# Performance work log

Hardware: AMD Instinct MI355X
Metric: run time of the kernel (lower is better)

## Reference

```python
import jax, jax.numpy as jnp
import numpy as np

H = 512          # lstm_hidden_size
NUM_OPS = 8
NUM_NODES = 4
TEMP = 5.0
TANH_C = 2.5
B = 4096
NUM_STEPS = 16   # 8 lstm steps x 2 decisions (node, op)


def setup_inputs() -> dict:
    key = jax.random.key(0)
    ks = jax.random.split(key, 20)
    u = lambda k, s: jax.random.uniform(k, s, jnp.float32, -0.1, 0.1)
    inp = {}
    # embedding: torch default init N(0,1)
    inp["emb"] = jax.random.normal(ks[0], (NUM_OPS + 1, H), jnp.float32)
    # LSTM (single layer), torch gate order i,f,g,o; init U(-0.1,0.1), bias 0
    inp["w_ih"] = u(ks[1], (4 * H, H))
    inp["w_hh"] = u(ks[2], (4 * H, H))
    inp["b_ih"] = jnp.zeros((4 * H,), jnp.float32)
    inp["b_hh"] = jnp.zeros((4 * H,), jnp.float32)
    # node-predecessor decoders: widths 2,3,4,5 (one per intermediate node)
    inp["wn2"] = u(ks[3], (2, H)); inp["bn2"] = jnp.zeros((2,), jnp.float32)
    inp["wn3"] = u(ks[4], (3, H)); inp["bn3"] = jnp.zeros((3,), jnp.float32)
    inp["wn4"] = u(ks[5], (4, H)); inp["bn4"] = jnp.zeros((4,), jnp.float32)
    inp["wn5"] = u(ks[6], (5, H)); inp["bn5"] = jnp.zeros((5,), jnp.float32)
    # op decoders: one [NUM_OPS, H] decoder per intermediate node
    inp["wop"] = u(ks[7], (NUM_NODES, NUM_OPS, H))
    inp["bop"] = jnp.zeros((NUM_NODES, NUM_OPS), jnp.float32)
    # Gumbel noise for multinomial sampling via Gumbel-max (padded to width 8)
    un = jax.random.uniform(ks[8], (NUM_STEPS, B, NUM_OPS), jnp.float32,
                            minval=1e-6, maxval=1.0 - 1e-6)
    inp["gumbel"] = -jnp.log(-jnp.log(un))
    inp["batch_size"] = B
    return inp


def _lstm_step(x, h, c, w_ih, w_hh, b_ih, b_hh):
    gates = x @ w_ih.T + h @ w_hh.T + b_ih + b_hh   # [B, 4H]
    i, f, g, o = jnp.split(gates, 4, axis=-1)
    i = jax.nn.sigmoid(i); f = jax.nn.sigmoid(f)
    g = jnp.tanh(g);       o = jax.nn.sigmoid(o)
    c = f * c + i * g
    h = o * jnp.tanh(c)
    return h, c


def _decide(logits, g):
    # logits: [B, k], g: [B, k] gumbel noise -> sample ~ softmax(logits)
    logp = jax.nn.log_softmax(logits, axis=-1)
    probs = jnp.exp(logp)
    action = jnp.argmax(logits + g, axis=-1)                     # [B]
    sel = jnp.take_along_axis(logp, action[:, None], 1)[:, 0]     # [B]
    ent = -(logp * probs).sum(-1)                                 # [B]
    return action, sel, ent


def reference(emb, w_ih, w_hh, b_ih, b_hh,
              wn2, bn2, wn3, bn3, wn4, bn4, wn5, bn5,
              wop, bop, gumbel, batch_size):
    node_dec = [(wn2, bn2), (wn3, bn3), (wn4, bn4), (wn5, bn5)]
    h = jnp.zeros((batch_size, H), emb.dtype)
    c = jnp.zeros((batch_size, H), emb.dtype)
    inputs = jnp.zeros((batch_size,), jnp.int32)   # initial token 0
    actions, log_probs, entropies = [], [], []
    step = 0
    for i in range(NUM_NODES):
        wn, bn = node_dec[i]
        k = wn.shape[0]
        for _ in range(2):  # two (prev_node, op) edges per node, one lstm step each
            x = emb[inputs]                                   # [B, H]
            h, c = _lstm_step(x, h, c, w_ih, w_hh, b_ih, b_hh)
            # node-predecessor decision: temperature + tanh squashing
            nl = TANH_C * jnp.tanh((h @ wn.T + bn) / TEMP)    # [B, k]
            a, s, e = _decide(nl, gumbel[step, :, :k])
            actions.append(a); log_probs.append(s); entropies.append(e)
            step += 1
            # op decision: temperature only (no tanh in original code)
            ol = (h @ wop[i].T + bop[i]) / TEMP               # [B, NUM_OPS]
            a, s, e = _decide(ol, gumbel[step])
            actions.append(a); log_probs.append(s); entropies.append(e)
            step += 1
            inputs = a  # op action feeds the next lstm step
    return (jnp.stack(actions).astype(jnp.int32),   # [16, B]
            jnp.stack(log_probs),                   # [16, B]
            jnp.stack(entropies))                   # [16, B]
```

## Files before the change

kernel.cpp:

```cpp
#include <hip/hip_runtime.h>


constexpr int Bsz = 4096;
constexpr int Hsz = 512;
constexpr int G4H = 2048;

typedef unsigned short ushort_t;
using short8 = __attribute__((ext_vector_type(8))) short;
using f32x4 = __attribute__((ext_vector_type(4))) float;

__device__ __forceinline__ ushort_t f2bf_hi(float f) {
  unsigned u = __float_as_uint(f);
  u += 0x7FFF + ((u >> 16) & 1);
  return (ushort_t)(u >> 16);
}
__device__ __forceinline__ float bf2f(ushort_t h) {
  return __uint_as_float((unsigned)h << 16);
}

__device__ __forceinline__ void glds16(const void* gsrc, void* ldst) {
  __builtin_amdgcn_global_load_lds(
      (const __attribute__((address_space(1))) void*)gsrc,
      (__attribute__((address_space(3))) void*)ldst, 16, 0, 0);
}

__global__ __launch_bounds__(256) void precompute_E(
    const float* __restrict__ emb, const float* __restrict__ w_ih,
    const float* __restrict__ b_ih, const float* __restrict__ b_hh,
    float* __restrict__ E, float* __restrict__ Eperm) {
  const int lane = threadIdx.x & 63;
  const int wid = (blockIdx.x << 2) + (threadIdx.x >> 6);
  const int t = wid >> 11;
  const int col = wid & 2047;
  const float* er = emb + (size_t)t * Hsz + (lane << 3);
  const float* wr = w_ih + (size_t)col * Hsz + (lane << 3);
  float4 e0 = *(const float4*)(er);
  float4 e1 = *(const float4*)(er + 4);
  float4 w0 = *(const float4*)(wr);
  float4 w1 = *(const float4*)(wr + 4);
  float v = e0.x * w0.x + e0.y * w0.y + e0.z * w0.z + e0.w * w0.w +
            e1.x * w1.x + e1.y * w1.y + e1.z * w1.z + e1.w * w1.w;
#pragma unroll
  for (int off = 32; off > 0; off >>= 1) v += __shfl_xor(v, off, 64);
  if (lane == 0) {
    float val = v + b_ih[col] + b_hh[col];
    E[wid] = val;
    int g = col >> 9, j = col & 511;
    Eperm[(size_t)t * G4H + (j << 2) + g] = val;
  }
}

__global__ __launch_bounds__(256) void build_wcat(
    const float* __restrict__ w_hh, ushort_t* __restrict__ Wcat) {
  int ct = blockIdx.y;
  int k = blockIdx.x * 256 + threadIdx.x;
  int j = ct >> 2, g = ct & 3;
  const float* srcrow = w_hh + (size_t)(g * 512 + j) * Hsz;
  ushort_t out;
  if (k < 512) {
    out = f2bf_hi(srcrow[k]);
  } else {
    float x = srcrow[k - 512];
    ushort_t hi = f2bf_hi(x);
    out = f2bf_hi(x - bf2f(hi));
  }
  Wcat[(size_t)ct * 1536 + k] = out;
}

__global__ __launch_bounds__(256) void class_gemm(
    const float* __restrict__ h, const float* __restrict__ w,
    float* __restrict__ G, int nq) {
  const int wid = (blockIdx.x << 2) + (threadIdx.x >> 6);
  const int lane = threadIdx.x & 63;
  const int q = wid >> 11;
  const int col = wid & 2047;
  if (q >= nq) return;
  const float* hr = h + (size_t)q * Hsz + (lane << 3);
  const float* wr = w + (size_t)col * Hsz + (lane << 3);
  float4 a0 = *(const float4*)(hr);
  float4 a1 = *(const float4*)(hr + 4);
  float4 b0 = *(const float4*)(wr);
  float4 b1 = *(const float4*)(wr + 4);
  float v = a0.x * b0.x + a0.y * b0.y + a0.z * b0.z + a0.w * b0.w +
            a1.x * b1.x + a1.y * b1.y + a1.z * b1.z + a1.w * b1.w;
#pragma unroll
  for (int off = 32; off > 0; off >>= 1) v += __shfl_xor(v, off, 64);
  if (lane == 0) G[(size_t)q * G4H + col] = v;
}

__global__ __launch_bounds__(256) void gemm64(
    const float* __restrict__ A, const float* __restrict__ Bw,
    float* __restrict__ G) {
  constexpr int LDA = 68;
  __shared__ float As[16 * LDA];
  __shared__ float Bs[16 * LDA];
  const int tid = threadIdx.x;
  const int bx = blockIdx.x & 31;
  const int by = blockIdx.x >> 5;
  const int r0 = by * 64, c0 = bx * 64;
  const int tx = tid & 15, ty = tid >> 4;
  const int lr = tid >> 2;
  const int lk = (tid & 3) << 2;
  const float* Ar = A + (size_t)(r0 + lr) * Hsz;
  const float* Br = Bw + (size_t)(c0 + lr) * Hsz;
  float acc[4][4];
#pragma unroll
  for (int i = 0; i < 4; ++i)
#pragma unroll
    for (int j = 0; j < 4; ++j) acc[i][j] = 0.0f;

  for (int k0 = 0; k0 < Hsz; k0 += 16) {
    float4 a = *(const float4*)(Ar + k0 + lk);
    float4 b = *(const float4*)(Br + k0 + lk);
    __syncthreads();
    As[(lk + 0) * LDA + lr] = a.x;
    As[(lk + 1) * LDA + lr] = a.y;
    As[(lk + 2) * LDA + lr] = a.z;
    As[(lk + 3) * LDA + lr] = a.w;
    Bs[(lk + 0) * LDA + lr] = b.x;
    Bs[(lk + 1) * LDA + lr] = b.y;
    Bs[(lk + 2) * LDA + lr] = b.z;
    Bs[(lk + 3) * LDA + lr] = b.w;
    __syncthreads();
#pragma unroll
    for (int kk = 0; kk < 16; ++kk) {
      float4 av = *(const float4*)&As[kk * LDA + (ty << 2)];
      float4 bv = *(const float4*)&Bs[kk * LDA + (tx << 2)];
      float avs[4] = {av.x, av.y, av.z, av.w};
      float bvs[4] = {bv.x, bv.y, bv.z, bv.w};
#pragma unroll
      for (int i = 0; i < 4; ++i)
#pragma unroll
        for (int j = 0; j < 4; ++j) acc[i][j] = fmaf(avs[i], bvs[j], acc[i][j]);
    }
  }
#pragma unroll
  for (int i = 0; i < 4; ++i)
#pragma unroll
    for (int j = 0; j < 4; ++j)
      G[(size_t)(r0 + (ty << 2) + i) * G4H + c0 + (tx << 2) + j] = acc[i][j];
}

__global__ __launch_bounds__(256) void step_pw(
    const float* __restrict__ G, const float* __restrict__ E,
    const float* __restrict__ c_prev, float* __restrict__ h_out,
    float* __restrict__ c_out, int nq) {
  int idx = blockIdx.x * 256 + threadIdx.x;
  if (idx >= nq * Hsz) return;
  int q = idx >> 9, j = idx & 511;
  int gq = q >> 3, er = q & 7;
  const float* Eg = E + (size_t)er * G4H;
  float iv = Eg[j], fv = Eg[512 + j], gv = Eg[1024 + j], ov = Eg[1536 + j];
  if (G) {
    const float* Gg = G + (size_t)gq * G4H;
    iv += Gg[j]; fv += Gg[512 + j]; gv += Gg[1024 + j]; ov += Gg[1536 + j];
  }
  float cp = c_prev ? c_prev[(size_t)gq * Hsz + j] : 0.0f;
  float ig = 1.0f / (1.0f + expf(-iv));
  float fg = 1.0f / (1.0f + expf(-fv));
  float gg = tanhf(gv);
  float og = 1.0f / (1.0f + expf(-ov));
  float cn = fg * cp + ig * gg;
  c_out[idx] = cn;
  h_out[idx] = og * tanhf(cn);
}

__global__ __launch_bounds__(256) void expand_pw(
    const float* __restrict__ G, const float* __restrict__ E,
    const float* __restrict__ c4, const int* __restrict__ cls3,
    const int* __restrict__ act3, float* __restrict__ h_out,
    float* __restrict__ c_out, ushort_t* __restrict__ Acat) {
  int idx = blockIdx.x * 256 + threadIdx.x;
  int r = idx >> 9, j = idx & 511;
  int q = cls3[r], er = act3[r];
  const float* Eg = E + (size_t)er * G4H;
  const float* Gg = G + (size_t)q * G4H;
  float iv = Gg[j] + Eg[j];
  float fv = Gg[512 + j] + Eg[512 + j];
  float gv = Gg[1024 + j] + Eg[1024 + j];
  float ov = Gg[1536 + j] + Eg[1536 + j];
  float cp = c4[(size_t)q * Hsz + j];
  float ig = 1.0f / (1.0f + expf(-iv));
  float fg = 1.0f / (1.0f + expf(-fv));
  float gg = tanhf(gv);
  float og = 1.0f / (1.0f + expf(-ov));
  float cn = fg * cp + ig * gg;
  float hn = og * tanhf(cn);
  c_out[idx] = cn;
  h_out[idx] = hn;
  ushort_t hi = f2bf_hi(hn);
  Acat[(size_t)r * 1024 + j] = hi;
  Acat[(size_t)r * 1024 + 512 + j] = f2bf_hi(hn - bf2f(hi));
}

__global__ __launch_bounds__(256) void gemm_bf16_lstm(
    const ushort_t* __restrict__ Acat, const ushort_t* __restrict__ Wcat,
    const float* __restrict__ Eperm, const int* __restrict__ act,
    float* __restrict__ cF, float* __restrict__ h_out,
    ushort_t* __restrict__ Aout) {
  __shared__ union {
    ushort_t P[2][4][128 * 32];
    float C[64 * 132];
  } sm;

  const int tid = threadIdx.x;
  const int wave = tid >> 6, lane = tid & 63;
  const int xcd = blockIdx.x & 7;
  const int i64 = blockIdx.x >> 3;
  const int by = ((xcd >> 1) << 3) + (i64 >> 3);
  const int bx = ((xcd & 1) << 3) + (i64 & 7);
  const int r0 = by * 128, c0 = bx * 128;
  const int wr = (wave >> 1) * 64, wc = (wave & 1) * 64;
  const int mrow = lane & 15, quad = lane >> 4;

  const int srow = lane >> 2;
  const int sk = (lane & 3) << 3;

  const ushort_t* sbase[8];
  int doff[8];
#pragma unroll
  for (int q = 0; q < 8; ++q) {
    const int g = (q << 2) + wave;
    const int panel = g >> 3;
    const int region = g & 7;
    const int row = region * 16 + srow;
    if (panel == 0)
      sbase[q] = Acat + (size_t)(r0 + row) * 1024 + sk;
    else if (panel == 1)
      sbase[q] = Acat + (size_t)(r0 + row) * 1024 + 512 + sk;
    else if (panel == 2)
      sbase[q] = Wcat + (size_t)(c0 + row) * 1536 + sk;
    else
      sbase[q] = Wcat + (size_t)(c0 + row) * 1536 + 512 + sk;
    doff[q] = panel * 8192 + region * 1024;
  }

  f32x4 acc[4][4];
#pragma unroll
  for (int i = 0; i < 4; ++i)
#pragma unroll
    for (int jt = 0; jt < 4; ++jt) acc[i][jt] = (f32x4){0.f, 0.f, 0.f, 0.f};

  auto stage = [&](int buf, int it) {
    const int ks = it << 5;
#pragma unroll
    for (int q = 0; q < 8; ++q)
      glds16(sbase[q] + ks, (char*)sm.P[0][0] + (buf << 15) + doff[q]);
  };

  stage(0, 0);
  __syncthreads();

  int cur = 0;
  for (int it = 0; it < 16; ++it) {
    if (it < 15) stage(cur ^ 1, it + 1);
    const ushort_t* AH = sm.P[cur][0];
    const ushort_t* AL = sm.P[cur][1];
    const ushort_t* BH = sm.P[cur][2];
    const ushort_t* BL = sm.P[cur][3];
    short8 ah[4], al[4], bh[4], bl[4];
#pragma unroll
    for (int i = 0; i < 4; ++i) {
      ah[i] = *(const short8*)&AH[(wr + i * 16 + mrow) * 32 + (quad << 3)];
      al[i] = *(const short8*)&AL[(wr + i * 16 + mrow) * 32 + (quad << 3)];
    }
#pragma unroll
    for (int jt = 0; jt < 4; ++jt) {
      bh[jt] = *(const short8*)&BH[(wc + jt * 16 + mrow) * 32 + (quad << 3)];
      bl[jt] = *(const short8*)&BL[(wc + jt * 16 + mrow) * 32 + (quad << 3)];
    }
#pragma unroll
    for (int i = 0; i < 4; ++i)
#pragma unroll
      for (int jt = 0; jt < 4; ++jt) {
        acc[i][jt] = __builtin_amdgcn_mfma_f32_16x16x32_bf16(
            ah[i], bh[jt], acc[i][jt], 0, 0, 0);
        acc[i][jt] = __builtin_amdgcn_mfma_f32_16x16x32_bf16(
            ah[i], bl[jt], acc[i][jt], 0, 0, 0);
        acc[i][jt] = __builtin_amdgcn_mfma_f32_16x16x32_bf16(
            al[i], bh[jt], acc[i][jt], 0, 0, 0);
      }
    __syncthreads();
    cur ^= 1;
  }

  const int jj = tid & 31;
  const int rbase = tid >> 5;
#pragma unroll
  for (int p = 0; p < 2; ++p) {
    __syncthreads();
    if ((wr >> 6) == p) {
#pragma unroll
      for (int i = 0; i < 4; ++i)
#pragma unroll
        for (int jt = 0; jt < 4; ++jt)
#pragma unroll
          for (int rg = 0; rg < 4; ++rg)
            sm.C[(i * 16 + quad * 4 + rg) * 132 + wc + jt * 16 + mrow] =
                acc[i][jt][rg];
    }
    __syncthreads();
#pragma unroll
    for (int rp = 0; rp < 8; ++rp) {
      const int rl = rbase * 8 + rp;
      const int grow = r0 + p * 64 + rl;
      float4 g4 = *(float4*)&sm.C[rl * 132 + jj * 4];
      const int a = act[grow];
      const int jglob = (c0 >> 2) + jj;
      float4 e4 = *(const float4*)&Eperm[(size_t)a * G4H + c0 + jj * 4];
      float iv = g4.x + e4.x, fv = g4.y + e4.y;
      float gv = g4.z + e4.z, ov = g4.w + e4.w;
      float ig = 1.0f / (1.0f + expf(-iv));
      float fg = 1.0f / (1.0f + expf(-fv));
      float gg = tanhf(gv);
      float og = 1.0f / (1.0f + expf(-ov));
      const size_t ci = (size_t)grow * Hsz + jglob;
      float cn = fg * cF[ci] + ig * gg;
      float hn = og * tanhf(cn);
      cF[ci] = cn;
      h_out[ci] = hn;
      ushort_t hi = f2bf_hi(hn);
      Aout[(size_t)grow * 1024 + jglob] = hi;
      Aout[(size_t)grow * 1024 + 512 + jglob] = f2bf_hi(hn - bf2f(hi));
    }
  }
}

template <int K>
__global__ __launch_bounds__(256) void decide_step(
    const float* __restrict__ h, const float* __restrict__ wn,
    const float* __restrict__ bn, const float* __restrict__ wopi,
    const float* __restrict__ bopi, const float* __restrict__ gum,
    float* __restrict__ oan, float* __restrict__ oao,
    float* __restrict__ oln, float* __restrict__ olo,
    float* __restrict__ oen, float* __restrict__ oeo,
    int* __restrict__ act_next, const int* __restrict__ hidx, int hmode,
    const int* __restrict__ cls_prev, int* __restrict__ cls_out) {
  const int lane = threadIdx.x & 63;
  const int r = (blockIdx.x << 2) + (threadIdx.x >> 6);
  const int idx = (hmode == 0) ? 0 : (hmode == 1 ? r : hidx[r]);
  const float* hr = h + (size_t)idx * Hsz;
  const float4 hv0 = *(const float4*)(hr + (lane << 3));
  const float4 hv1 = *(const float4*)(hr + (lane << 3) + 4);

  float nl[K];
#pragma unroll
  for (int j = 0; j < K; ++j) {
    const float* w = wn + (size_t)j * Hsz;
    float4 w0 = *(const float4*)(w + (lane << 3));
    float4 w1 = *(const float4*)(w + (lane << 3) + 4);
    float v = hv0.x * w0.x + hv0.y * w0.y + hv0.z * w0.z + hv0.w * w0.w +
              hv1.x * w1.x + hv1.y * w1.y + hv1.z * w1.z + hv1.w * w1.w;
#pragma unroll
    for (int off = 32; off > 0; off >>= 1) v += __shfl_xor(v, off, 64);
    nl[j] = 2.5f * tanhf((v + bn[j]) / 5.0f);
  }
  float ol[8];
#pragma unroll
  for (int j = 0; j < 8; ++j) {
    const float* w = wopi + (size_t)j * Hsz;
    float4 w0 = *(const float4*)(w + (lane << 3));
    float4 w1 = *(const float4*)(w + (lane << 3) + 4);
    float v = hv0.x * w0.x + hv0.y * w0.y + hv0.z * w0.z + hv0.w * w0.w +
              hv1.x * w1.x + hv1.y * w1.y + hv1.z * w1.z + hv1.w * w1.w;
#pragma unroll
    for (int off = 32; off > 0; off >>= 1) v += __shfl_xor(v, off, 64);
    ol[j] = (v + bopi[j]) / 5.0f;
  }

  {
    const float* g = gum + (size_t)r * 8;
    float m = nl[0];
#pragma unroll
    for (int j = 1; j < K; ++j) m = fmaxf(m, nl[j]);
    float se = 0.0f;
#pragma unroll
    for (int j = 0; j < K; ++j) se += expf(nl[j] - m);
    float lse = logf(se);
    int a = 0;
    float best = nl[0] + g[0];
#pragma unroll
    for (int j = 1; j < K; ++j) {
      float v = nl[j] + g[j];
      if (v > best) { best = v; a = j; }
    }
    float ent = 0.0f, sel = 0.0f;
#pragma unroll
    for (int j = 0; j < K; ++j) {
      float lp = nl[j] - m - lse;
      ent -= lp * expf(lp);
      if (j == a) sel = lp;
    }
    if (lane == 0) { oan[r] = (float)a; oln[r] = sel; oen[r] = ent; }
  }
  {
    const float* g = gum + (size_t)Bsz * 8 + (size_t)r * 8;
    float m = ol[0];
#pragma unroll
    for (int j = 1; j < 8; ++j) m = fmaxf(m, ol[j]);
    float se = 0.0f;
#pragma unroll
    for (int j = 0; j < 8; ++j) se += expf(ol[j] - m);
    float lse = logf(se);
    int a = 0;
    float best = ol[0] + g[0];
#pragma unroll
    for (int j = 1; j < 8; ++j) {
      float v = ol[j] + g[j];
      if (v > best) { best = v; a = j; }
    }
    float ent = 0.0f, sel = 0.0f;
#pragma unroll
    for (int j = 0; j < 8; ++j) {
      float lp = ol[j] - m - lse;
      ent -= lp * expf(lp);
      if (j == a) sel = lp;
    }
    if (lane == 0) {
      oao[r] = (float)a; olo[r] = sel; oeo[r] = ent;
      act_next[r] = a;
      if (cls_out) cls_out[r] = (cls_prev ? cls_prev[r] * 8 : 0) + a;
    }
  }
}

extern "C" void kernel_launch(void* const* d_in, const int* in_sizes, int n_in,
                              void* d_out, int out_size, void* d_ws,
                              size_t ws_size, hipStream_t stream) {
  (void)in_sizes; (void)n_in; (void)out_size; (void)ws_size;
  const float* emb = (const float*)d_in[0];
  const float* w_ih = (const float*)d_in[1];
  const float* w_hh = (const float*)d_in[2];
  const float* b_ih = (const float*)d_in[3];
  const float* b_hh = (const float*)d_in[4];
  const float* wn[4] = {(const float*)d_in[5], (const float*)d_in[7],
                        (const float*)d_in[9], (const float*)d_in[11]};
  const float* bn[4] = {(const float*)d_in[6], (const float*)d_in[8],
                        (const float*)d_in[10], (const float*)d_in[12]};
  const float* wop = (const float*)d_in[13];
  const float* bop = (const float*)d_in[14];
  const float* gum = (const float*)d_in[15];

  float* ws = (float*)d_ws;
  float* E = ws;                 ws += 9 * G4H;
  float* Eperm = ws;             ws += 9 * G4H;
  float* h1 = ws;                ws += Hsz;
  float* c1 = ws;                ws += Hsz;
  float* h2 = ws;                ws += 8 * Hsz;
  float* c2 = ws;                ws += 8 * Hsz;
  float* h3 = ws;                ws += 64 * Hsz;
  float* c3 = ws;                ws += 64 * Hsz;
  float* h4 = ws;                ws += 512 * Hsz;
  float* c4 = ws;                ws += 512 * Hsz;
  float* Gearly = ws;
  ushort_t* AcatB = (ushort_t*)Gearly;
  ws += (8u << 20) / 4;
  ushort_t* AcatA = (ushort_t*)ws;      ws += (8u << 20) / 4;
  ushort_t* Wcat = (ushort_t*)ws;       ws += (6u << 20) / 4;
  float* hA = ws;                ws += (size_t)Bsz * Hsz;
  float* cF = ws;                ws += (size_t)Bsz * Hsz;
  int* act = (int*)ws;
  int* cls = act + Bsz;

  float* out = (float*)d_out;
  const size_t SZ = (size_t)16 * Bsz;

  auto decide = [&](int s, const float* h, int hmode, const int* hidx,
                    const int* cls_prev, int* cls_out) {
    const int i = s >> 1;
    float* oan = out + (size_t)(2 * s) * Bsz;
    float* oao = out + (size_t)(2 * s + 1) * Bsz;
    float* oln = out + SZ + (size_t)(2 * s) * Bsz;
    float* olo = out + SZ + (size_t)(2 * s + 1) * Bsz;
    float* oen = out + 2 * SZ + (size_t)(2 * s) * Bsz;
    float* oeo = out + 2 * SZ + (size_t)(2 * s + 1) * Bsz;
    const float* gn = gum + (size_t)(2 * s) * Bsz * 8;
    const float* wopi = wop + (size_t)i * 8 * Hsz;
    const float* bopi = bop + (size_t)i * 8;
    switch (i) {
      case 0:
        decide_step<2><<<Bsz / 4, 256, 0, stream>>>(h, wn[0], bn[0], wopi, bopi,
            gn, oan, oao, oln, olo, oen, oeo, act, hidx, hmode, cls_prev, cls_out);
        break;
      case 1:
        decide_step<3><<<Bsz / 4, 256, 0, stream>>>(h, wn[1], bn[1], wopi, bopi,
            gn, oan, oao, oln, olo, oen, oeo, act, hidx, hmode, cls_prev, cls_out);
        break;
      case 2:
        decide_step<4><<<Bsz / 4, 256, 0, stream>>>(h, wn[2], bn[2], wopi, bopi,
            gn, oan, oao, oln, olo, oen, oeo, act, hidx, hmode, cls_prev, cls_out);
        break;
      default:
        decide_step<5><<<Bsz / 4, 256, 0, stream>>>(h, wn[3], bn[3], wopi, bopi,
            gn, oan, oao, oln, olo, oen, oeo, act, hidx, hmode, cls_prev, cls_out);
        break;
    }
  };

  precompute_E<<<(9 * G4H) / 4, 256, 0, stream>>>(emb, w_ih, b_ih, b_hh, E,
                                                  Eperm);
  build_wcat<<<dim3(4, 2048), 256, 0, stream>>>(w_hh, Wcat);

  step_pw<<<2, 256, 0, stream>>>(nullptr, E, nullptr, h1, c1, 1);
  decide(0, h1, 0, nullptr, nullptr, cls);

  class_gemm<<<512, 256, 0, stream>>>(h1, w_hh, Gearly, 1);
  step_pw<<<16, 256, 0, stream>>>(Gearly, E, c1, h2, c2, 8);
  decide(1, h2, 2, cls, cls, cls);

  class_gemm<<<4096, 256, 0, stream>>>(h2, w_hh, Gearly, 8);
  step_pw<<<128, 256, 0, stream>>>(Gearly, E, c2, h3, c3, 64);
  decide(2, h3, 2, cls, cls, cls);

  gemm64<<<32, 256, 0, stream>>>(h3, w_hh, Gearly);
  step_pw<<<1024, 256, 0, stream>>>(Gearly, E, c3, h4, c4, 512);
  decide(3, h4, 2, cls, nullptr, nullptr);

  gemm64<<<256, 256, 0, stream>>>(h4, w_hh, Gearly);
  expand_pw<<<(Bsz * Hsz) / 256, 256, 0, stream>>>(Gearly, E, c4, cls, act, hA,
                                                   cF, AcatA);
  decide(4, hA, 1, nullptr, nullptr, nullptr);

  ushort_t* ain = AcatA;
  ushort_t* aout = AcatB;
  for (int s = 5; s < 8; ++s) {
    gemm_bf16_lstm<<<512, 256, 0, stream>>>(ain, Wcat, Eperm, act, cF, hA, aout);
    decide(s, hA, 1, nullptr, nullptr, nullptr);
    ushort_t* t = ain; ain = aout; aout = t;
  }
}
```

Before: 395.0 us.

## Fuse LSTM early-step pointwise, GEMM epilogues and decisions to cut launches

Merges precompute_E and build_wcat into one setup launch. Folds the first LSTM step into its decision kernel and the next two steps into warp-level matvec kernels. Moves the pointwise cell update into the GEMM epilogue with a gate-permuted weight row order, and fuses step 4's expand into its decision kernel. The aim is to remove many small kernel launches and intermediate gate buffers on the serial early steps. In exchange some threads recompute h1 redundantly and lanes sit idle in the small fused kernels.

Result: slower. 434.2 us (+9.9%).

```diff
diff --git a/kernel.cpp b/kernel.cpp
--- a/kernel.cpp
+++ b/kernel.cpp
@@ -17,6 +17,9 @@
 __device__ __forceinline__ float bf2f(ushort_t h) {
   return __uint_as_float((unsigned)h << 16);
 }
+__device__ __forceinline__ float sigf(float x) {
+  return 1.0f / (1.0f + expf(-x));
+}
 
 __device__ __forceinline__ void glds16(const void* gsrc, void* ldst) {
   __builtin_amdgcn_global_load_lds(
@@ -24,73 +27,269 @@
       (__attribute__((address_space(3))) void*)ldst, 16, 0, 0);
 }
 
-__global__ __launch_bounds__(256) void precompute_E(
+__global__ __launch_bounds__(256) void setup_fused(
     const float* __restrict__ emb, const float* __restrict__ w_ih,
     const float* __restrict__ b_ih, const float* __restrict__ b_hh,
-    float* __restrict__ E, float* __restrict__ Eperm) {
+    const float* __restrict__ w_hh, float* __restrict__ Eperm,
+    ushort_t* __restrict__ Wcat) {
+  if (blockIdx.x < 4608) {
+    const int lane = threadIdx.x & 63;
+    const int wid = (blockIdx.x << 2) + (threadIdx.x >> 6);
+    const int t = wid >> 11;
+    const int col = wid & 2047;
+    const float* er = emb + (size_t)t * Hsz + (lane << 3);
+    const float* wr = w_ih + (size_t)col * Hsz + (lane << 3);
+    float4 e0 = *(const float4*)(er);
+    float4 e1 = *(const float4*)(er + 4);
+    float4 w0 = *(const float4*)(wr);
+    float4 w1 = *(const float4*)(wr + 4);
+    float v = e0.x * w0.x + e0.y * w0.y + e0.z * w0.z + e0.w * w0.w +
+              e1.x * w1.x + e1.y * w1.y + e1.z * w1.z + e1.w * w1.w;
+#pragma unroll
+    for (int off = 32; off > 0; off >>= 1) v += __shfl_xor(v, off, 64);
+    if (lane == 0) {
+      float val = v + b_ih[col] + b_hh[col];
+      Eperm[(size_t)t * G4H + ((col & 511) << 2) + (col >> 9)] = val;
+    }
+  } else {
+    const int b = blockIdx.x - 4608;
+    const int ct = b >> 2;
+    const int k = ((b & 3) << 8) + threadIdx.x;
+    const int j = ct >> 2, g = ct & 3;
+    const float* srcrow = w_hh + (size_t)(g * 512 + j) * Hsz;
+    ushort_t out;
+    if (k < 512) {
+      out = f2bf_hi(srcrow[k]);
+    } else {
+      float x = srcrow[k - 512];
+      ushort_t hi = f2bf_hi(x);
+      out = f2bf_hi(x - bf2f(hi));
+    }
+    Wcat[(size_t)ct * 1536 + k] = out;
+  }
+}
+
+template <int K>
+__device__ __forceinline__ void decide_core(
+    const float4 hv0, const float4 hv1, const int lane, const int r,
+    const float* __restrict__ wn, const float* __restrict__ bn,
+    const float* __restrict__ wopi, const float* __restrict__ bopi,
+    const float* __restrict__ gum, float* __restrict__ oan,
+    float* __restrict__ oao, float* __restrict__ oln, float* __restrict__ olo,
+    float* __restrict__ oen, float* __restrict__ oeo,
+    int* __restrict__ act_next, const int* __restrict__ cls_prev,
+    int* __restrict__ cls_out) {
+  float nl[K];
+#pragma unroll
+  for (int j = 0; j < K; ++j) {
+    const float* w = wn + (size_t)j * Hsz;
+    float4 w0 = *(const float4*)(w + (lane << 3));
+    float4 w1 = *(const float4*)(w + (lane << 3) + 4);
+    float v = hv0.x * w0.x + hv0.y * w0.y + hv0.z * w0.z + hv0.w * w0.w +
+              hv1.x * w1.x + hv1.y * w1.y + hv1.z * w1.z + hv1.w * w1.w;
+#pragma unroll
+    for (int off = 32; off > 0; off >>= 1) v += __shfl_xor(v, off, 64);
+    nl[j] = 2.5f * tanhf((v + bn[j]) / 5.0f);
+  }
+  float ol[8];
+#pragma unroll
+  for (int j = 0; j < 8; ++j) {
+    const float* w = wopi + (size_t)j * Hsz;
+    float4 w0 = *(const float4*)(w + (lane << 3));
+    float4 w1 = *(const float4*)(w + (lane << 3) + 4);
+    float v = hv0.x * w0.x + hv0.y * w0.y + hv0.z * w0.z + hv0.w * w0.w +
+              hv1.x * w1.x + hv1.y * w1.y + hv1.z * w1.z + hv1.w * w1.w;
+#pragma unroll
+    for (int off = 32; off > 0; off >>= 1) v += __shfl_xor(v, off, 64);
+    ol[j] = (v + bopi[j]) / 5.0f;
+  }
+
+  {
+    const float* g = gum + (size_t)r * 8;
+    float m = nl[0];
+#pragma unroll
+    for (int j = 1; j < K; ++j) m = fmaxf(m, nl[j]);
+    float se = 0.0f;
+#pragma unroll
+    for (int j = 0; j < K; ++j) se += expf(nl[j] - m);
+    float lse = logf(se);
+    int a = 0;
+    float best = nl[0] + g[0];
+#pragma unroll
+    for (int j = 1; j < K; ++j) {
+      float v = nl[j] + g[j];
+      if (v > best) { best = v; a = j; }
+    }
+    float ent = 0.0f, sel = 0.0f;
+#pragma unroll
+    for (int j = 0; j < K; ++j) {
+      float lp = nl[j] - m - lse;
+      ent -= lp * expf(lp);
+      if (j == a) sel = lp;
+    }
+    if (lane == 0) { oan[r] = (float)a; oln[r] = sel; oen[r] = ent; }
+  }
+  {
+    const float* g = gum + (size_t)Bsz * 8 + (size_t)r * 8;
+    float m = ol[0];
+#pragma unroll
+    for (int j = 1; j < 8; ++j) m = fmaxf(m, ol[j]);
+    float se = 0.0f;
+#pragma unroll
+    for (int j = 0; j < 8; ++j) se += expf(ol[j] - m);
+    float lse = logf(se);
+    int a = 0;
+    float best = ol[0] + g[0];
+#pragma unroll
+    for (int j = 1; j < 8; ++j) {
+      float v = ol[j] + g[j];
+      if (v > best) { best = v; a = j; }
+    }
+    float ent = 0.0f, sel = 0.0f;
+#pragma unroll
+    for (int j = 0; j < 8; ++j) {
+      float lp = ol[j] - m - lse;
+      ent -= lp * expf(lp);
+      if (j == a) sel = lp;
+    }
+    if (lane == 0) {
+      oao[r] = (float)a; olo[r] = sel; oeo[r] = ent;
+      act_next[r] = a;
+      if (cls_out) cls_out[r] = (cls_prev ? cls_prev[r] * 8 : 0) + a;
+    }
+  }
+}
+
+template <int K>
+__global__ __launch_bounds__(256) void decide_step(
+    const float* __restrict__ h, const float* __restrict__ wn,
+    const float* __restrict__ bn, const float* __restrict__ wopi,
+    const float* __restrict__ bopi, const float* __restrict__ gum,
+    float* __restrict__ oan, float* __restrict__ oao,
+    float* __restrict__ oln, float* __restrict__ olo,
+    float* __restrict__ oen, float* __restrict__ oeo,
+    int* __restrict__ act_next, const int* __restrict__ hidx, int hmode,
+    const int* __restrict__ cls_prev, int* __restrict__ cls_out) {
+  const int lane = threadIdx.x & 63;
+  const int r = (blockIdx.x << 2) + (threadIdx.x >> 6);
+  const int idx = (hmode == 1) ? r : hidx[r];
+  const float* hr = h + (size_t)idx * Hsz;
+  const float4 hv0 = *(const float4*)(hr + (lane << 3));
+  const float4 hv1 = *(const float4*)(hr + (lane << 3) + 4);
+  decide_core<K>(hv0, hv1, lane, r, wn, bn, wopi, bopi, gum, oan, oao, oln,
+                 olo, oen, oeo, act_next, cls_prev, cls_out);
+}
+
+__global__ __launch_bounds__(256) void decide0_step(
+    const float* __restrict__ Eperm, const float* __restrict__ wn,
+    const float* __restrict__ bn, const float* __restrict__ wopi,
+    const float* __restrict__ bopi, const float* __restrict__ gum,
+    float* __restrict__ oan, float* __restrict__ oao,
+    float* __restrict__ oln, float* __restrict__ olo,
+    float* __restrict__ oen, float* __restrict__ oeo,
+    int* __restrict__ act_next, int* __restrict__ cls_out) {
+  const int lane = threadIdx.x & 63;
+  const int r = (blockIdx.x << 2) + (threadIdx.x >> 6);
+  float h8[8];
+#pragma unroll
+  for (int kk = 0; kk < 8; ++kk) {
+    float4 e = *(const float4*)&Eperm[(size_t)(((lane << 3) + kk) << 2)];
+    float ig = sigf(e.x);
+    float gg = tanhf(e.z);
+    float og = sigf(e.w);
+    float cn = ig * gg;
+    h8[kk] = og * tanhf(cn);
+  }
+  float4 hv0 = {h8[0], h8[1], h8[2], h8[3]};
+  float4 hv1 = {h8[4], h8[5], h8[6], h8[7]};
+  decide_core<2>(hv0, hv1, lane, r, wn, bn, wopi, bopi, gum, oan, oao, oln,
+                 olo, oen, oeo, act_next, nullptr, cls_out);
+}
+
+__global__ __launch_bounds__(256) void fused_step1(
+    const float* __restrict__ Eperm, const float* __restrict__ w_hh,
+    float* __restrict__ h2, float* __restrict__ c2) {
+  const int lane = threadIdx.x & 63;
+  const int j = (blockIdx.x << 2) + (threadIdx.x >> 6);
+  float h8[8];
+#pragma unroll
+  for (int kk = 0; kk < 8; ++kk) {
+    float4 e = *(const float4*)&Eperm[(size_t)(((lane << 3) + kk) << 2)];
+    h8[kk] = sigf(e.w) * tanhf(sigf(e.x) * tanhf(e.z));
+  }
+  float v[4];
+#pragma unroll
+  for (int g = 0; g < 4; ++g) {
+    const float* w = w_hh + (size_t)(g * 512 + j) * Hsz + (lane << 3);
+    float4 w0 = *(const float4*)(w);
+    float4 w1 = *(const float4*)(w + 4);
+    v[g] = h8[0] * w0.x + h8[1] * w0.y + h8[2] * w0.z + h8[3] * w0.w +
+           h8[4] * w1.x + h8[5] * w1.y + h8[6] * w1.z + h8[7] * w1.w;
+  }
+#pragma unroll
+  for (int off = 32; off > 0; off >>= 1) {
+#pragma unroll
+    for (int g = 0; g < 4; ++g) v[g] += __shfl_xor(v[g], off, 64);
+  }
+  float4 e0 = *(const float4*)&Eperm[(size_t)(j << 2)];
+  float c1j = sigf(e0.x) * tanhf(e0.z);
+  if (lane < 8) {
+    const int er = lane;
+    float4 e = *(const float4*)&Eperm[(size_t)er * G4H + (j << 2)];
+    float ig = sigf(v[0] + e.x);
+    float fg = sigf(v[1] + e.y);
+    float gg = tanhf(v[2] + e.z);
+    float og = sigf(v[3] + e.w);
+    float cn = fg * c1j + ig * gg;
+    h2[er * Hsz + j] = og * tanhf(cn);
+    c2[er * Hsz + j] = cn;
+  }
+}
+
+__global__ __launch_bounds__(256) void fused_step2(
+    const float* __restrict__ Eperm, const float* __restrict__ w_hh,
+    const float* __restrict__ h2, const float* __restrict__ c2,
+    float* __restrict__ h3, float* __restrict__ c3) {
   const int lane = threadIdx.x & 63;
   const int wid = (blockIdx.x << 2) + (threadIdx.x >> 6);
-  const int t = wid >> 11;
-  const int col = wid & 2047;
-  const float* er = emb + (size_t)t * Hsz + (lane << 3);
-  const float* wr = w_ih + (size_t)col * Hsz + (lane << 3);
-  float4 e0 = *(const float4*)(er);
-  float4 e1 = *(const float4*)(er + 4);
-  float4 w0 = *(const float4*)(wr);
-  float4 w1 = *(const float4*)(wr + 4);
-  float v = e0.x * w0.x + e0.y * w0.y + e0.z * w0.z + e0.w * w0.w +
-            e1.x * w1.x + e1.y * w1.y + e1.z * w1.z + e1.w * w1.w;
-#pragma unroll
-  for (int off = 32; off > 0; off >>= 1) v += __shfl_xor(v, off, 64);
-  if (lane == 0) {
-    float val = v + b_ih[col] + b_hh[col];
-    E[wid] = val;
-    int g = col >> 9, j = col & 511;
-    Eperm[(size_t)t * G4H + (j << 2) + g] = val;
-  }
-}
-
-__global__ __launch_bounds__(256) void build_wcat(
-    const float* __restrict__ w_hh, ushort_t* __restrict__ Wcat) {
-  int ct = blockIdx.y;
-  int k = blockIdx.x * 256 + threadIdx.x;
-  int j = ct >> 2, g = ct & 3;
-  const float* srcrow = w_hh + (size_t)(g * 512 + j) * Hsz;
-  ushort_t out;
-  if (k < 512) {
-    out = f2bf_hi(srcrow[k]);
-  } else {
-    float x = srcrow[k - 512];
-    ushort_t hi = f2bf_hi(x);
-    out = f2bf_hi(x - bf2f(hi));
-  }
-  Wcat[(size_t)ct * 1536 + k] = out;
-}
-
-__global__ __launch_bounds__(256) void class_gemm(
-    const float* __restrict__ h, const float* __restrict__ w,
-    float* __restrict__ G, int nq) {
-  const int wid = (blockIdx.x << 2) + (threadIdx.x >> 6);
-  const int lane = threadIdx.x & 63;
-  const int q = wid >> 11;
-  const int col = wid & 2047;
-  if (q >= nq) return;
-  const float* hr = h + (size_t)q * Hsz + (lane << 3);
-  const float* wr = w + (size_t)col * Hsz + (lane << 3);
+  const int gq = wid >> 9, j = wid & 511;
+  const float* hr = h2 + (size_t)gq * Hsz + (lane << 3);
   float4 a0 = *(const float4*)(hr);
   float4 a1 = *(const float4*)(hr + 4);
-  float4 b0 = *(const float4*)(wr);
-  float4 b1 = *(const float4*)(wr + 4);
-  float v = a0.x * b0.x + a0.y * b0.y + a0.z * b0.z + a0.w * b0.w +
-            a1.x * b1.x + a1.y * b1.y + a1.z * b1.z + a1.w * b1.w;
-#pragma unroll
-  for (int off = 32; off > 0; off >>= 1) v += __shfl_xor(v, off, 64);
-  if (lane == 0) G[(size_t)q * G4H + col] = v;
-}
-
-__global__ __launch_bounds__(256) void gemm64(
-    const float* __restrict__ A, const float* __restrict__ Bw,
-    float* __restrict__ G) {
+  float v[4];
+#pragma unroll
+  for (int g = 0; g < 4; ++g) {
+    const float* w = w_hh + (size_t)(g * 512 + j) * Hsz + (lane << 3);
+    float4 w0 = *(const float4*)(w);
+    float4 w1 = *(const float4*)(w + 4);
+    v[g] = a0.x * w0.x + a0.y * w0.y + a0.z * w0.z + a0.w * w0.w +
+           a1.x * w1.x + a1.y * w1.y + a1.z * w1.z + a1.w * w1.w;
+  }
+#pragma unroll
+  for (int off = 32; off > 0; off >>= 1) {
+#pragma unroll
+    for (int g = 0; g < 4; ++g) v[g] += __shfl_xor(v[g], off, 64);
+  }
+  float cp = c2[(size_t)gq * Hsz + j];
+  if (lane < 8) {
+    const int er = lane;
+    float4 e = *(const float4*)&Eperm[(size_t)er * G4H + (j << 2)];
+    float ig = sigf(v[0] + e.x);
+    float fg = sigf(v[1] + e.y);
+    float gg = tanhf(v[2] + e.z);
+    float og = sigf(v[3] + e.w);
+    float cn = fg * cp + ig * gg;
+    h3[(size_t)((gq << 3) + er) * Hsz + j] = og * tanhf(cn);
+    c3[(size_t)((gq << 3) + er) * Hsz + j] = cn;
+  }
+}
+
+template <int MODE>
+__global__ __launch_bounds__(256) void gemm64ct(
+    const float* __restrict__ A, const float* __restrict__ w_hh,
+    const float* __restrict__ Eperm, const float* __restrict__ c_in,
+    float* __restrict__ Gperm, float* __restrict__ h_o,
+    float* __restrict__ c_o) {
   constexpr int LDA = 68;
   __shared__ float As[16 * LDA];
   __shared__ float Bs[16 * LDA];
@@ -101,8 +300,10 @@
   const int tx = tid & 15, ty = tid >> 4;
   const int lr = tid >> 2;
   const int lk = (tid & 3) << 2;
+  const int ct = c0 + lr;
+  const int brow = (ct & 3) * 512 + (ct >> 2);
   const float* Ar = A + (size_t)(r0 + lr) * Hsz;
-  const float* Br = Bw + (size_t)(c0 + lr) * Hsz;
+  const float* Br = w_hh + (size_t)brow * Hsz;
   float acc[4][4];
 #pragma unroll
   for (int i = 0; i < 4; ++i)
@@ -134,63 +335,71 @@
         for (int j = 0; j < 4; ++j) acc[i][j] = fmaf(avs[i], bvs[j], acc[i][j]);
     }
   }
-#pragma unroll
-  for (int i = 0; i < 4; ++i)
-#pragma unroll
-    for (int j = 0; j < 4; ++j)
-      G[(size_t)(r0 + (ty << 2) + i) * G4H + c0 + (tx << 2) + j] = acc[i][j];
-}
-
-__global__ __launch_bounds__(256) void step_pw(
-    const float* __restrict__ G, const float* __restrict__ E,
-    const float* __restrict__ c_prev, float* __restrict__ h_out,
-    float* __restrict__ c_out, int nq) {
-  int idx = blockIdx.x * 256 + threadIdx.x;
-  if (idx >= nq * Hsz) return;
-  int q = idx >> 9, j = idx & 511;
-  int gq = q >> 3, er = q & 7;
-  const float* Eg = E + (size_t)er * G4H;
-  float iv = Eg[j], fv = Eg[512 + j], gv = Eg[1024 + j], ov = Eg[1536 + j];
-  if (G) {
-    const float* Gg = G + (size_t)gq * G4H;
-    iv += Gg[j]; fv += Gg[512 + j]; gv += Gg[1024 + j]; ov += Gg[1536 + j];
-  }
-  float cp = c_prev ? c_prev[(size_t)gq * Hsz + j] : 0.0f;
-  float ig = 1.0f / (1.0f + expf(-iv));
-  float fg = 1.0f / (1.0f + expf(-fv));
-  float gg = tanhf(gv);
-  float og = 1.0f / (1.0f + expf(-ov));
-  float cn = fg * cp + ig * gg;
-  c_out[idx] = cn;
-  h_out[idx] = og * tanhf(cn);
-}
-
-__global__ __launch_bounds__(256) void expand_pw(
-    const float* __restrict__ G, const float* __restrict__ E,
-    const float* __restrict__ c4, const int* __restrict__ cls3,
-    const int* __restrict__ act3, float* __restrict__ h_out,
-    float* __restrict__ c_out, ushort_t* __restrict__ Acat) {
-  int idx = blockIdx.x * 256 + threadIdx.x;
-  int r = idx >> 9, j = idx & 511;
-  int q = cls3[r], er = act3[r];
-  const float* Eg = E + (size_t)er * G4H;
-  const float* Gg = G + (size_t)q * G4H;
-  float iv = Gg[j] + Eg[j];
-  float fv = Gg[512 + j] + Eg[512 + j];
-  float gv = Gg[1024 + j] + Eg[1024 + j];
-  float ov = Gg[1536 + j] + Eg[1536 + j];
-  float cp = c4[(size_t)q * Hsz + j];
-  float ig = 1.0f / (1.0f + expf(-iv));
-  float fg = 1.0f / (1.0f + expf(-fv));
-  float gg = tanhf(gv);
-  float og = 1.0f / (1.0f + expf(-ov));
-  float cn = fg * cp + ig * gg;
-  float hn = og * tanhf(cn);
-  c_out[idx] = cn;
-  h_out[idx] = hn;
-  ushort_t hi = f2bf_hi(hn);
-  Acat[(size_t)r * 1024 + j] = hi;
-  Acat[(size_t)r * 1024 + 512 + j] = f2bf_hi(hn - bf2f(hi));
+  const int jcol = (c0 >> 2) + tx;
+  if (MODE == 0) {
+#pragma unroll
+    for (int i = 0; i < 4; ++i) {
+      float4 o = {acc[i][0], acc[i][1], acc[i][2], acc[i][3]};
+      *(float4*)&Gperm[(size_t)(r0 + (ty << 2) + i) * G4H + (jcol << 2)] = o;
+    }
+  } else {
+#pragma unroll
+    for (int i = 0; i < 4; ++i) {
+      const int q = r0 + (ty << 2) + i;
+      float cp = c_in[(size_t)q * Hsz + jcol];
+#pragma unroll
+      for (int er = 0; er < 8; ++er) {
+        float4 e = *(const float4*)&Eperm[(size_t)er * G4H + (jcol << 2)];
+        float ig = sigf(acc[i][0] + e.x);
+        float fg = sigf(acc[i][1] + e.y);
+        float gg = tanhf(acc[i][2] + e.z);
+        float og = sigf(acc[i][3] + e.w);
+        float cn = fg * cp + ig * gg;
+        h_o[(size_t)((q << 3) + er) * Hsz + jcol] = og * tanhf(cn);
+        c_o[(size_t)((q << 3) + er) * Hsz + jcol] = cn;
+      }
+    }
+  }
+}
+
+__global__ __launch_bounds__(256) void decide4_fused(
+    const float* __restrict__ Gperm, const float* __restrict__ Eperm,
+    const float* __restrict__ c4, const int* __restrict__ cls,
+    float* __restrict__ cF, ushort_t* __restrict__ Acat,
+    const float* __restrict__ wn, const float* __restrict__ bn,
+    const float* __restrict__ wopi, const float* __restrict__ bopi,
+    const float* __restrict__ gum, float* __restrict__ oan,
+    float* __restrict__ oao, float* __restrict__ oln, float* __restrict__ olo,
+    float* __restrict__ oen, float* __restrict__ oeo,
+    int* __restrict__ act) {
+  const int lane = threadIdx.x & 63;
+  const int r = (blockIdx.x << 2) + (threadIdx.x >> 6);
+  const int q = cls[r];
+  const int er = act[r];
+  const float* Gr = Gperm + (size_t)q * G4H;
+  const float* Er = Eperm + (size_t)er * G4H;
+  float h8[8];
+#pragma unroll
+  for (int kk = 0; kk < 8; ++kk) {
+    const int j = (lane << 3) + kk;
+    float4 g4 = *(const float4*)&Gr[j << 2];
+    float4 e4 = *(const float4*)&Er[j << 2];
+    float ig = sigf(g4.x + e4.x);
+    float fg = sigf(g4.y + e4.y);
+    float gg = tanhf(g4.z + e4.z);
+    float og = sigf(g4.w + e4.w);
+    float cn = fg * c4[(size_t)q * Hsz + j] + ig * gg;
+    float hn = og * tanhf(cn);
+    cF[(size_t)r * Hsz + j] = cn;
+    h8[kk] = hn;
+    ushort_t hi = f2bf_hi(hn);
+    Acat[(size_t)r * 1024 + j] = hi;
+    Acat[(size_t)r * 1024 + 512 + j] = f2bf_hi(hn - bf2f(hi));
+  }
+  float4 hv0 = {h8[0], h8[1], h8[2], h8[3]};
+  float4 hv1 = {h8[4], h8[5], h8[6], h8[7]};
+  decide_core<4>(hv0, hv1, lane, r, wn, bn, wopi, bopi, gum, oan, oao, oln,
+                 olo, oen, oeo, act, nullptr, nullptr);
 }
 
 __global__ __launch_bounds__(256) void gemm_bf16_lstm(
@@ -326,104 +535,6 @@
   }
 }
 
-template <int K>
-__global__ __launch_bounds__(256) void decide_step(
-    const float* __restrict__ h, const float* __restrict__ wn,
-    const float* __restrict__ bn, const float* __restrict__ wopi,
-    const float* __restrict__ bopi, const float* __restrict__ gum,
-    float* __restrict__ oan, float* __restrict__ oao,
-    float* __restrict__ oln, float* __restrict__ olo,
-    float* __restrict__ oen, float* __restrict__ oeo,
-    int* __restrict__ act_next, const int* __restrict__ hidx, int hmode,
-    const int* __restrict__ cls_prev, int* __restrict__ cls_out) {
-  const int lane = threadIdx.x & 63;
-  const int r = (blockIdx.x << 2) + (threadIdx.x >> 6);
-  const int idx = (hmode == 0) ? 0 : (hmode == 1 ? r : hidx[r]);
-  const float* hr = h + (size_t)idx * Hsz;
-  const float4 hv0 = *(const float4*)(hr + (lane << 3));
-  const float4 hv1 = *(const float4*)(hr + (lane << 3) + 4);
-
-  float nl[K];
-#pragma unroll
-  for (int j = 0; j < K; ++j) {
-    const float* w = wn + (size_t)j * Hsz;
-    float4 w0 = *(const float4*)(w + (lane << 3));
-    float4 w1 = *(const float4*)(w + (lane << 3) + 4);
-    float v = hv0.x * w0.x + hv0.y * w0.y + hv0.z * w0.z + hv0.w * w0.w +
-              hv1.x * w1.x + hv1.y * w1.y + hv1.z * w1.z + hv1.w * w1.w;
-#pragma unroll
-    for (int off = 32; off > 0; off >>= 1) v += __shfl_xor(v, off, 64);
-    nl[j] = 2.5f * tanhf((v + bn[j]) / 5.0f);
-  }
-  float ol[8];
-#pragma unroll
-  for (int j = 0; j < 8; ++j) {
-    const float* w = wopi + (size_t)j * Hsz;
-    float4 w0 = *(const float4*)(w + (lane << 3));
-    float4 w1 = *(const float4*)(w + (lane << 3) + 4);
-    float v = hv0.x * w0.x + hv0.y * w0.y + hv0.z * w0.z + hv0.w * w0.w +
-              hv1.x * w1.x + hv1.y * w1.y + hv1.z * w1.z + hv1.w * w1.w;
-#pragma unroll
-    for (int off = 32; off > 0; off >>= 1) v += __shfl_xor(v, off, 64);
-    ol[j] = (v + bopi[j]) / 5.0f;
-  }
-
-  {
-    const float* g = gum + (size_t)r * 8;
-    float m = nl[0];
-#pragma unroll
-    for (int j = 1; j < K; ++j) m = fmaxf(m, nl[j]);
-    float se = 0.0f;
-#pragma unroll
-    for (int j = 0; j < K; ++j) se += expf(nl[j] - m);
-    float lse = logf(se);
-    int a = 0;
-    float best = nl[0] + g[0];
-#pragma unroll
-    for (int j = 1; j < K; ++j) {
-      float v = nl[j] + g[j];
-      if (v > best) { best = v; a = j; }
-    }
-    float ent = 0.0f, sel = 0.0f;
-#pragma unroll
-    for (int j = 0; j < K; ++j) {
-      float lp = nl[j] - m - lse;
-      ent -= lp * expf(lp);
-      if (j == a) sel = lp;
-    }
-    if (lane == 0) { oan[r] = (float)a; oln[r] = sel; oen[r] = ent; }
-  }
-  {
-    const float* g = gum + (size_t)Bsz * 8 + (size_t)r * 8;
-    float m = ol[0];
-#pragma unroll
-    for (int j = 1; j < 8; ++j) m = fmaxf(m, ol[j]);
-    float se = 0.0f;
-#pragma unroll
-    for (int j = 0; j < 8; ++j) se += expf(ol[j] - m);
-    float lse = logf(se);
-    int a = 0;
-    float best = ol[0] + g[0];
-#pragma unroll
-    for (int j = 1; j < 8; ++j) {
-      float v = ol[j] + g[j];
-      if (v > best) { best = v; a = j; }
-    }
-    float ent = 0.0f, sel = 0.0f;
-#pragma unroll
-    for (int j = 0; j < 8; ++j) {
-      float lp = ol[j] - m - lse;
-      ent -= lp * expf(lp);
-      if (j == a) sel = lp;
-    }
-    if (lane == 0) {
-      oao[r] = (float)a; olo[r] = sel; oeo[r] = ent;
-      act_next[r] = a;
-      if (cls_out) cls_out[r] = (cls_prev ? cls_prev[r] * 8 : 0) + a;
-    }
-  }
-}
-
 extern "C" void kernel_launch(void* const* d_in, const int* in_sizes, int n_in,
                               void* d_out, int out_size, void* d_ws,
                               size_t ws_size, hipStream_t stream) {
@@ -442,18 +553,15 @@
   const float* gum = (const float*)d_in[15];
 
   float* ws = (float*)d_ws;
-  float* E = ws;                 ws += 9 * G4H;
   float* Eperm = ws;             ws += 9 * G4H;
-  float* h1 = ws;                ws += Hsz;
-  float* c1 = ws;                ws += Hsz;
   float* h2 = ws;                ws += 8 * Hsz;
   float* c2 = ws;                ws += 8 * Hsz;
   float* h3 = ws;                ws += 64 * Hsz;
   float* c3 = ws;                ws += 64 * Hsz;
   float* h4 = ws;                ws += 512 * Hsz;
   float* c4 = ws;                ws += 512 * Hsz;
-  float* Gearly = ws;
-  ushort_t* AcatB = (ushort_t*)Gearly;
+  float* Gperm = ws;
+  ushort_t* AcatB = (ushort_t*)Gperm;
   ws += (8u << 20) / 4;
   ushort_t* AcatA = (ushort_t*)ws;      ws += (8u << 20) / 4;
   ushort_t* Wcat = (ushort_t*)ws;       ws += (6u << 20) / 4;
@@ -465,16 +573,23 @@
   float* out = (float*)d_out;
   const size_t SZ = (size_t)16 * Bsz;
 
+  auto outp = [&](int s, float*& oan, float*& oao, float*& oln, float*& olo,
+                  float*& oen, float*& oeo, const float*& gn) {
+    oan = out + (size_t)(2 * s) * Bsz;
+    oao = out + (size_t)(2 * s + 1) * Bsz;
+    oln = out + SZ + (size_t)(2 * s) * Bsz;
+    olo = out + SZ + (size_t)(2 * s + 1) * Bsz;
+    oen = out + 2 * SZ + (size_t)(2 * s) * Bsz;
+    oeo = out + 2 * SZ + (size_t)(2 * s + 1) * Bsz;
+    gn = gum + (size_t)(2 * s) * Bsz * 8;
+  };
+
   auto decide = [&](int s, const float* h, int hmode, const int* hidx,
                     const int* cls_prev, int* cls_out) {
     const int i = s >> 1;
-    float* oan = out + (size_t)(2 * s) * Bsz;
-    float* oao = out + (size_t)(2 * s + 1) * Bsz;
-    float* oln = out + SZ + (size_t)(2 * s) * Bsz;
-    float* olo = out + SZ + (size_t)(2 * s + 1) * Bsz;
-    float* oen = out + 2 * SZ + (size_t)(2 * s) * Bsz;
-    float* oeo = out + 2 * SZ + (size_t)(2 * s + 1) * Bsz;
-    const float* gn = gum + (size_t)(2 * s) * Bsz * 8;
+    float *oan, *oao, *oln, *olo, *oen, *oeo;
+    const float* gn;
+    outp(s, oan, oao, oln, olo, oen, oeo, gn);
     const float* wopi = wop + (size_t)i * 8 * Hsz;
     const float* bopi = bop + (size_t)i * 8;
     switch (i) {
@@ -497,29 +612,36 @@
     }
   };
 
-  precompute_E<<<(9 * G4H) / 4, 256, 0, stream>>>(emb, w_ih, b_ih, b_hh, E,
-                                                  Eperm);
-  build_wcat<<<dim3(4, 2048), 256, 0, stream>>>(w_hh, Wcat);
-
-  step_pw<<<2, 256, 0, stream>>>(nullptr, E, nullptr, h1, c1, 1);
-  decide(0, h1, 0, nullptr, nullptr, cls);
-
-  class_gemm<<<512, 256, 0, stream>>>(h1, w_hh, Gearly, 1);
-  step_pw<<<16, 256, 0, stream>>>(Gearly, E, c1, h2, c2, 8);
+  setup_fused<<<4608 + 8192, 256, 0, stream>>>(emb, w_ih, b_ih, b_hh, w_hh,
+                                               Eperm, Wcat);
+
+  {
+    float *oan, *oao, *oln, *olo, *oen, *oeo;
+    const float* gn;
+    outp(0, oan, oao, oln, olo, oen, oeo, gn);
+    decide0_step<<<Bsz / 4, 256, 0, stream>>>(Eperm, wn[0], bn[0], wop, bop,
+        gn, oan, oao, oln, olo, oen, oeo, act, cls);
+  }
+
+  fused_step1<<<128, 256, 0, stream>>>(Eperm, w_hh, h2, c2);
   decide(1, h2, 2, cls, cls, cls);
 
-  class_gemm<<<4096, 256, 0, stream>>>(h2, w_hh, Gearly, 8);
-  step_pw<<<128, 256, 0, stream>>>(Gearly, E, c2, h3, c3, 64);
+  fused_step2<<<1024, 256, 0, stream>>>(Eperm, w_hh, h2, c2, h3, c3);
   decide(2, h3, 2, cls, cls, cls);
 
-  gemm64<<<32, 256, 0, stream>>>(h3, w_hh, Gearly);
-  step_pw<<<1024, 256, 0, stream>>>(Gearly, E, c3, h4, c4, 512);
+  gemm64ct<1><<<32, 256, 0, stream>>>(h3, w_hh, Eperm, c3, nullptr, h4, c4);
   decide(3, h4, 2, cls, nullptr, nullptr);
 
-  gemm64<<<256, 256, 0, stream>>>(h4, w_hh, Gearly);
-  expand_pw<<<(Bsz * Hsz) / 256, 256, 0, stream>>>(Gearly, E, c4, cls, act, hA,
-                                                   cF, AcatA);
-  decide(4, hA, 1, nullptr, nullptr, nullptr);
+  gemm64ct<0><<<256, 256, 0, stream>>>(h4, w_hh, nullptr, nullptr, Gperm,
+                                       nullptr, nullptr);
+  {
+    float *oan, *oao, *oln, *olo, *oen, *oeo;
+    const float* gn;
+    outp(4, oan, oao, oln, olo, oen, oeo, gn);
+    decide4_fused<<<Bsz / 4, 256, 0, stream>>>(Gperm, Eperm, c4, cls, cF,
+        AcatA, wn[2], bn[2], wop + (size_t)2 * 8 * Hsz, bop + 2 * 8, gn,
+        oan, oao, oln, olo, oen, oeo, act);
+  }
 
   ushort_t* ain = AcatA;
   ushort_t* aout = AcatB;
```
